# Kernel tuning notes

Hardware: AMD Instinct MI355X
Metric: run time of the kernel (lower is better)

The kernel has to match this reference:

```python
import jax, jax.numpy as jnp
import numpy as np

B, S, H = 32768, 16, 16  # batch, seq_len, G_hiddensize (code requires H == S and H == latent_dim == 16)
LATENT = 16
DISC_DIMS = [(1, 32), (32, 16), (16, 8), (8, 16), (16, 32)]


def setup_inputs() -> dict:
    key = jax.random.key(0)
    ks = iter(jax.random.split(key, 64))
    def p(shape, scale=0.1):
        return (jax.random.normal(next(ks), shape, dtype=jnp.float32) * scale)
    inp = dict(
        values=jax.random.normal(next(ks), (B, S), dtype=jnp.float32),
        masks=jax.random.randint(next(ks), (B, S), 0, 2).astype(jnp.int32),
        g_fwd_Wih=p((4 * H, 1)), g_fwd_Whh=p((4 * H, H)), g_fwd_b=p((4 * H,)),
        g_bwd_Wih=p((4 * H, 1)), g_bwd_Whh=p((4 * H, H)), g_bwd_b=p((4 * H,)),
        imp_W=p((1, H)), imp_b=p((1,)),
        fc_W=p((LATENT, H)), fc_b=p((LATENT,)),
        dec_Wih=p((4 * H, LATENT)), dec_Whh=p((4 * H, H)), dec_b=p((4 * H,)),
        dec_out_W=p((1, H)), dec_out_b=p((1,)),
        disc_out_W=p((1, 32)), disc_out_b=p((1,)),
    )
    for k, (i, h) in enumerate(DISC_DIMS):
        inp[f"d_W_{k}"] = p((4 * h, i))
        inp[f"d_b_{k}"] = p((4 * h,))
    return inp


def lstm_cell(x, h, c, Wih, Whh, b):
    gates = x @ Wih.T + h @ Whh.T + b
    i, f, g, o = jnp.split(gates, 4, axis=-1)
    c = jax.nn.sigmoid(f) * c + jax.nn.sigmoid(i) * jnp.tanh(g)
    h = jax.nn.sigmoid(o) * jnp.tanh(c)
    return h, c


def _forward(values, masks, g_fwd_Wih, g_fwd_Whh, g_fwd_b, g_bwd_Wih, g_bwd_Whh, g_bwd_b,
             imp_W, imp_b, fc_W, fc_b, dec_Wih, dec_Whh, dec_b, dec_out_W, dec_out_b,
             disc_out_W, disc_out_b,
             d_W_0, d_b_0, d_W_1, d_b_1, d_W_2, d_b_2, d_W_3, d_b_3, d_W_4, d_b_4):
    dt = values.dtype
    Bsz = values.shape[0]
    x = values[:, :, None]                     # (B, S, 1)
    m = masks.astype(dt)[:, :, None]           # (B, S, 1)
    # NOTE: torch.flip along axis 2 (size 1) is a no-op, so the bwd cell sees the
    # same (un-reversed) sequence as the fwd cell -- faithfully reproduced here.
    zH = jnp.zeros((Bsz, H), dt)
    h_f, c_f = lstm_cell(jnp.full((Bsz, 1), 128.0, dt), zH, zH, g_fwd_Wih, g_fwd_Whh, g_fwd_b)
    h_b, c_b = lstm_cell(jnp.full((Bsz, 1), -128.0, dt), zH, zH, g_bwd_Wih, g_bwd_Whh, g_bwd_b)

    def gen_step(carry, xm):
        h_f, c_f, h_b, c_b = carry
        x_t, m_t = xm                          # (B,1) each
        cc_f = (1 - m_t) * x_t + m_t * (h_f @ imp_W.T + imp_b)
        cc_b = (1 - m_t) * x_t + m_t * (h_b @ imp_W.T + imp_b)
        h_f, c_f = lstm_cell(cc_f, h_f, c_f, g_fwd_Wih, g_fwd_Whh, g_fwd_b)
        h_b, c_b = lstm_cell(cc_b, h_b, c_b, g_bwd_Wih, g_bwd_Whh, g_bwd_b)
        return (h_f, c_f, h_b, c_b), None

    (h_f, c_f, h_b, c_b), _ = jax.lax.scan(
        gen_step, (h_f, c_f, h_b, c_b),
        (jnp.transpose(x, (1, 0, 2)), jnp.transpose(m, (1, 0, 2))))
    h = h_f + h_b                               # (B, H), H == S
    imputations = h.reshape(Bsz, S, 1)
    imputed = imputations * (1 - m) + x * m      # (B, S, 1)

    # Discriminator: torch calls each LSTMCell WITHOUT state every timestep, so
    # hidden/cell start at zero each call -> purely feedforward per (batch, t).
    # W_hh @ 0 == 0, so only W_ih and the combined bias matter. Vectorize over B*S.
    inp = imputed.reshape(Bsz * S, 1)
    for W, b in ((d_W_0, d_b_0), (d_W_1, d_b_1), (d_W_2, d_b_2), (d_W_3, d_b_3), (d_W_4, d_b_4)):
        gates = inp @ W.T + b
        i, f, g, o = jnp.split(gates, 4, axis=-1)
        cc = jax.nn.sigmoid(i) * jnp.tanh(g)
        inp = jax.nn.sigmoid(o) * jnp.tanh(cc)
    disc_output = (inp @ disc_out_W.T + disc_out_b).reshape(Bsz, S, 1)

    latent = h @ fc_W.T + fc_b                  # (B, 16)

    # Decoder: ignores latent values (only uses batch size); start token = 128s.
    hd = cd = jnp.zeros((Bsz, H), dt)
    hd, cd = lstm_cell(jnp.full((Bsz, LATENT), 128.0, dt), hd, cd, dec_Wih, dec_Whh, dec_b)

    def dec_step(carry, _):
        hd, cd = carry
        hd, cd = lstm_cell(cd, hd, cd, dec_Wih, dec_Whh, dec_b)
        return (hd, cd), hd @ dec_out_W.T + dec_out_b

    _, outs = jax.lax.scan(dec_step, (hd, cd), None, length=S)  # (S, B, 1)
    reconstructed = jnp.transpose(outs, (1, 0, 2))
    return imputed, disc_output, latent, reconstructed


def reference(values, masks, g_fwd_Wih, g_fwd_Whh, g_fwd_b, g_bwd_Wih, g_bwd_Whh, g_bwd_b,
              imp_W, imp_b, fc_W, fc_b, dec_Wih, dec_Whh, dec_b, dec_out_W, dec_out_b,
              disc_out_W, disc_out_b,
              d_W_0, d_b_0, d_W_1, d_b_1, d_W_2, d_b_2, d_W_3, d_b_3, d_W_4, d_b_4):
    return _forward(values, masks, g_fwd_Wih, g_fwd_Whh, g_fwd_b, g_bwd_Wih, g_bwd_Whh, g_bwd_b,
                    imp_W, imp_b, fc_W, fc_b, dec_Wih, dec_Whh, dec_b, dec_out_W, dec_out_b,
                    disc_out_W, disc_out_b,
                    d_W_0, d_b_0, d_W_1, d_b_1, d_W_2, d_b_2, d_W_3, d_b_3, d_W_4, d_b_4)
```

## Files before the change

### kernel.cpp

```cpp
#include <hip/hip_runtime.h>

#define BB 32768
#define BS (BB*16)

typedef __attribute__((ext_vector_type(8))) short bf8v;
typedef __attribute__((ext_vector_type(4))) float f4v;

#define RECO 64
#define TAB  128
#define NTAB 2049
#define HFO  8448
#define HBO  (HFO+BS)

#define PW0 0
#define PB0 96
#define PW1 192
#define PB1 1920
#define PW2 1968
#define PB2 2448
#define PW3 2472
#define PB3 3048
#define PW4 3096
#define PB4 5016
#define POW 5112
#define POB 5144
#define PNU 5148

#define SMF 2580

#define NSCAN 256
#define NTABB 129

__device__ __forceinline__ float sigm(float x){
    return __builtin_amdgcn_rcpf(1.f + __expf(-x));
}
__device__ __forceinline__ float tanh_f(float x){
    return 1.f - 2.f * __builtin_amdgcn_rcpf(1.f + __expf(2.f * x));
}
__device__ __forceinline__ float dunit(float gi, float gg, float go){
    return sigm(go) * tanh_f(sigm(gi) * tanh_f(gg));
}
__device__ __forceinline__ unsigned short f2bf(float f){
    union { float f; unsigned int i; } v; v.f = f;
    unsigned int x = v.i;
    unsigned int r = x + 0x7fffu + ((x >> 16) & 1u);
    return (unsigned short)(r >> 16);
}
__device__ __forceinline__ float bfu(unsigned short s){
    union { unsigned u; float f; } v; v.u = ((unsigned)s) << 16; return v.f;
}
__device__ __forceinline__ float bflo(unsigned p){
    union { unsigned u; float f; } v; v.u = p << 16; return v.f;
}
__device__ __forceinline__ float bfhi(unsigned p){
    union { unsigned u; float f; } v; v.u = p & 0xffff0000u; return v.f;
}

struct P29 { const float* p[29]; };

__device__ __forceinline__ bf8v makeB(const float* Whh, const float* Wih,
                                      int row, int quad)
{
    bf8v B = {0,0,0,0,0,0,0,0};
    if (quad < 2) {
        const float4* p = (const float4*)(Whh + row*16 + quad*8);
        float4 a0 = p[0], a1 = p[1];
        B[0]=(short)f2bf(a0.x); B[1]=(short)f2bf(a0.y);
        B[2]=(short)f2bf(a0.z); B[3]=(short)f2bf(a0.w);
        B[4]=(short)f2bf(a1.x); B[5]=(short)f2bf(a1.y);
        B[6]=(short)f2bf(a1.z); B[7]=(short)f2bf(a1.w);
    } else if (quad == 2) {
        B[0] = (short)f2bf(Wih[row]);
    }
    return B;
}

__global__ __launch_bounds__(256, 1)
void k_main(P29 a, const int* __restrict__ masks, float* __restrict__ ws)
{
    __shared__ __align__(16) float smem[SMF];
    int tid = threadIdx.x;

    if (blockIdx.x < NSCAN) {
        int lane = tid & 63;
        int wv   = tid >> 6;
        int m    = lane & 15;
        int quad = lane >> 4;
        int dir  = (int)(blockIdx.x >= 128);
        int b0   = (blockIdx.x & 127) * 256 + wv * 64;

        const float* __restrict__ Wih = a.p[2 + 3*dir];
        const float* __restrict__ Whh = a.p[3 + 3*dir];
        const float* __restrict__ bia = a.p[4 + 3*dir];

        bf8v Ai = makeB(Whh, Wih, m,      quad);
        bf8v Af = makeB(Whh, Wih, 16+m,   quad);
        bf8v Ag = makeB(Whh, Wih, 32+m,   quad);
        bf8v Ao = makeB(Whh, Wih, 48+m,   quad);
        bf8v Ap = {0,0,0,0,0,0,0,0};
        if (quad < 2) {
            const float4* p = (const float4*)(a.p[8] + quad*8);
            float4 a0 = p[0], a1 = p[1];
            Ap[0]=(short)f2bf(a0.x); Ap[1]=(short)f2bf(a0.y);
            Ap[2]=(short)f2bf(a0.z); Ap[3]=(short)f2bf(a0.w);
            Ap[4]=(short)f2bf(a1.x); Ap[5]=(short)f2bf(a1.y);
            Ap[6]=(short)f2bf(a1.z); Ap[7]=(short)f2bf(a1.w);
        }
        float impb = a.p[9][0];
        const f4v cz = {0.f, 0.f, 0.f, 0.f};

        f4v cbi, cbf, cbg, cbo;
        {
            float4 t;
            t = *(const float4*)(bia +      quad*4); cbi = (f4v){t.x,t.y,t.z,t.w};
            t = *(const float4*)(bia + 16 + quad*4); cbf = (f4v){t.x,t.y,t.z,t.w};
            t = *(const float4*)(bia + 32 + quad*4); cbg = (f4v){t.x,t.y,t.z,t.w};
            t = *(const float4*)(bia + 48 + quad*4); cbo = (f4v){t.x,t.y,t.z,t.w};
        }

        float sgn = dir ? -128.f : 128.f;
        float c[4][4], hl[4][4];
        {
            float4 wI = *(const float4*)(Wih +      quad*4);
            float4 wG = *(const float4*)(Wih + 32 + quad*4);
            float4 wO = *(const float4*)(Wih + 48 + quad*4);
            float wIv[4] = {wI.x, wI.y, wI.z, wI.w};
            float wGv[4] = {wG.x, wG.y, wG.z, wG.w};
            float wOv[4] = {wO.x, wO.y, wO.z, wO.w};
            #pragma unroll
            for (int r = 0; r < 4; r++) {
                float gi0 = sgn*wIv[r] + cbi[r];
                float gg0 = sgn*wGv[r] + cbg[r];
                float go0 = sgn*wOv[r] + cbo[r];
                float c0 = sigm(gi0) * tanh_f(gg0);
                float h0 = sigm(go0) * tanh_f(c0);
                #pragma unroll
                for (int s = 0; s < 4; s++) { c[s][r] = c0; hl[s][r] = h0; }
            }
        }
        unsigned u01[4], u23[4];
        #pragma unroll
        for (int s = 0; s < 4; s++) {
            asm("v_cvt_pk_bf16_f32 %0, %1, %2" : "=v"(u01[s]) : "v"(hl[s][0]), "v"(hl[s][1]));
            asm("v_cvt_pk_bf16_f32 %0, %1, %2" : "=v"(u23[s]) : "v"(hl[s][2]), "v"(hl[s][3]));
        }

        int pa0 = ((m + quad*32)      & 63) << 2;
        int pa1 = ((m + quad*32 + 16) & 63) << 2;

        const float* xr[4];
        const int*   mr[4];
        #pragma unroll
        for (int s = 0; s < 4; s++) {
            xr[s] = a.p[0] + (size_t)(b0 + 16*s + m) * 16;
            mr[s] = masks  + (size_t)(b0 + 16*s + m) * 16;
        }

        #pragma unroll 1
        for (int t4 = 0; t4 < 4; t4++) {
            float xa[4][4];
            int   ma[4][4];
            #pragma unroll
            for (int s = 0; s < 4; s++) {
                float4 xv = *(const float4*)(xr[s] + t4*4);
                int4   mv = *(const int4*)(mr[s] + t4*4);
                xa[s][0]=xv.x; xa[s][1]=xv.y; xa[s][2]=xv.z; xa[s][3]=xv.w;
                ma[s][0]=mv.x; ma[s][1]=mv.y; ma[s][2]=mv.z; ma[s][3]=mv.w;
            }
            #pragma unroll
            for (int j = 0; j < 4; j++) {
                union U4 { int i[4]; bf8v v; } B[4];
                #pragma unroll
                for (int s = 0; s < 4; s++) {
                    int w0 = __builtin_amdgcn_ds_bpermute(pa0, (int)u01[s]);
                    int w1 = __builtin_amdgcn_ds_bpermute(pa0, (int)u23[s]);
                    int w2 = __builtin_amdgcn_ds_bpermute(pa1, (int)u01[s]);
                    int w3 = __builtin_amdgcn_ds_bpermute(pa1, (int)u23[s]);
                    bool hi2 = quad >= 2;
                    B[s].i[0] = hi2 ? 0 : w0;
                    B[s].i[1] = hi2 ? 0 : w1;
                    B[s].i[2] = hi2 ? 0 : w2;
                    B[s].i[3] = hi2 ? 0 : w3;
                }
                #pragma unroll
                for (int s = 0; s < 4; s++) {
                    f4v dimp = __builtin_amdgcn_mfma_f32_16x16x32_bf16(Ap, B[s].v, cz, 0, 0, 0);
                    float cc = ma[s][j] ? (dimp[0] + impb) : xa[s][j];
                    unsigned ccw;
                    asm("v_cvt_pk_bf16_f32 %0, %1, %2" : "=v"(ccw) : "v"(cc), "v"(0.f));
                    if (quad == 2) B[s].i[0] = (int)ccw;
                    f4v di  = __builtin_amdgcn_mfma_f32_16x16x32_bf16(Ai, B[s].v, cbi, 0, 0, 0);
                    f4v df_ = __builtin_amdgcn_mfma_f32_16x16x32_bf16(Af, B[s].v, cbf, 0, 0, 0);
                    f4v dg  = __builtin_amdgcn_mfma_f32_16x16x32_bf16(Ag, B[s].v, cbg, 0, 0, 0);
                    f4v dO  = __builtin_amdgcn_mfma_f32_16x16x32_bf16(Ao, B[s].v, cbo, 0, 0, 0);
                    #pragma unroll
                    for (int r = 0; r < 4; r++) {
                        float cn = sigm(df_[r])*c[s][r] + sigm(di[r])*tanh_f(dg[r]);
                        c[s][r] = cn;
                        hl[s][r] = sigm(dO[r])*tanh_f(cn);
                    }
                    asm("v_cvt_pk_bf16_f32 %0, %1, %2" : "=v"(u01[s]) : "v"(hl[s][0]), "v"(hl[s][1]));
                    asm("v_cvt_pk_bf16_f32 %0, %1, %2" : "=v"(u23[s]) : "v"(hl[s][2]), "v"(hl[s][3]));
                }
            }
        }
        float* outp = ws + HFO + (size_t)dir*BS + (size_t)b0*16;
        #pragma unroll
        for (int s = 0; s < 4; s++)
            #pragma unroll
            for (int r = 0; r < 4; r++)
                outp[(16*s + m)*16 + quad*4 + r] = hl[s][r];
        return;
    }

    if (blockIdx.x < NSCAN + NTABB) {
        unsigned short* wl = (unsigned short*)smem;
#define STAGE(WS, BSi, h, K, padK, wdst, bdst) \
    { const float* Wp = a.p[WS]; const float* Bp2 = a.p[BSi]; \
      for (int i = tid; i < 3*(h)*(K); i += 256){ \
        int r = i/(K), k = i - r*(K); int g = r/(h), u0 = r - g*(h); \
        int sr = (g==0? u0 : (g==1? 2*(h)+u0 : 3*(h)+u0)); \
        wl[(wdst) + r*(padK) + k] = f2bf(Wp[sr*(K) + k]); } \
      for (int i = tid; i < 3*(h); i += 256){ \
        int g = i/(h), u0 = i - g*(h); \
        int sr = (g==0? u0 : (g==1? 2*(h)+u0 : 3*(h)+u0)); \
        wl[(bdst) + i] = f2bf(Bp2[sr]); } }
        STAGE(19, 20, 32,  1,  1, PW0, PB0)
        STAGE(21, 22, 16, 32, 36, PW1, PB1)
        STAGE(23, 24,  8, 16, 20, PW2, PB2)
        STAGE(25, 26, 16,  8, 12, PW3, PB3)
        STAGE(27, 28, 32, 16, 20, PW4, PB4)
#undef STAGE
        { const float* s = a.p[17]; for (int i = tid; i < 32; i += 256) wl[POW+i] = f2bf(s[i]); }
        if (tid == 0) wl[POB] = f2bf(a.p[18][0]);
        __syncthreads();
        int u = tid & 15;
        int gbase = (tid & 63) & 48;
        int gid = (blockIdx.x - NSCAN) * 16 + (tid >> 4);
        const uint2* w2 = (const uint2*)wl;
        float xin = -8.f + (float)gid * (1.f/128.f);
        float lo = dunit(xin*bfu(wl[PW0+u])    + bfu(wl[PB0+u]),
                         xin*bfu(wl[PW0+32+u]) + bfu(wl[PB0+32+u]),
                         xin*bfu(wl[PW0+64+u]) + bfu(wl[PB0+64+u]));
        float hi = dunit(xin*bfu(wl[PW0+16+u]) + bfu(wl[PB0+16+u]),
                         xin*bfu(wl[PW0+48+u]) + bfu(wl[PB0+48+u]),
                         xin*bfu(wl[PW0+80+u]) + bfu(wl[PB0+80+u]));
        float A0[32];
        #pragma unroll
        for (int k = 0; k < 16; k++) { A0[k] = __shfl(lo, gbase+k); A0[16+k] = __shfl(hi, gbase+k); }
        float gi = bfu(wl[PB1+u]), gg = bfu(wl[PB1+16+u]), go = bfu(wl[PB1+32+u]);
        int bi_ = (PW1 + u*36)>>2, bg_ = (PW1 + (16+u)*36)>>2, bo_ = (PW1 + (32+u)*36)>>2;
        #pragma unroll
        for (int q = 0; q < 8; q++) {
            uint2 wi = w2[bi_+q], wg = w2[bg_+q], wo = w2[bo_+q];
            float b0=A0[4*q], b1=A0[4*q+1], b2=A0[4*q+2], b3=A0[4*q+3];
            gi += b0*bflo(wi.x) + b1*bfhi(wi.x) + b2*bflo(wi.y) + b3*bfhi(wi.y);
            gg += b0*bflo(wg.x) + b1*bfhi(wg.x) + b2*bflo(wg.y) + b3*bfhi(wg.y);
            go += b0*bflo(wo.x) + b1*bfhi(wo.x) + b2*bflo(wo.y) + b3*bfhi(wo.y);
        }
        float a1 = dunit(gi, gg, go);
        float A1[16];
        #pragma unroll
        for (int k = 0; k < 16; k++) A1[k] = __shfl(a1, gbase+k);
        int v = u & 7;
        gi = bfu(wl[PB2+v]); gg = bfu(wl[PB2+8+v]); go = bfu(wl[PB2+16+v]);
        bi_ = (PW2 + v*20)>>2; bg_ = (PW2 + (8+v)*20)>>2; bo_ = (PW2 + (16+v)*20)>>2;
        #pragma unroll
        for (int q = 0; q < 4; q++) {
            uint2 wi = w2[bi_+q], wg = w2[bg_+q], wo = w2[bo_+q];
            float b0=A1[4*q], b1=A1[4*q+1], b2=A1[4*q+2], b3=A1[4*q+3];
            gi += b0*bflo(wi.x) + b1*bfhi(wi.x) + b2*bflo(wi.y) + b3*bfhi(wi.y);
            gg += b0*bflo(wg.x) + b1*bfhi(wg.x) + b2*bflo(wg.y) + b3*bfhi(wg.y);
            go += b0*bflo(wo.x) + b1*bfhi(wo.x) + b2*bflo(wo.y) + b3*bfhi(wo.y);
        }
        float a2 = dunit(gi, gg, go);
        float A2[8];
        #pragma unroll
        for (int k = 0; k < 8; k++) A2[k] = __shfl(a2, gbase+k);
        gi = bfu(wl[PB3+u]); gg = bfu(wl[PB3+16+u]); go = bfu(wl[PB3+32+u]);
        bi_ = (PW3 + u*12)>>2; bg_ = (PW3 + (16+u)*12)>>2; bo_ = (PW3 + (32+u)*12)>>2;
        #pragma unroll
        for (int q = 0; q < 2; q++) {
            uint2 wi = w2[bi_+q], wg = w2[bg_+q], wo = w2[bo_+q];
            float b0=A2[4*q], b1=A2[4*q+1], b2=A2[4*q+2], b3=A2[4*q+3];
            gi += b0*bflo(wi.x) + b1*bfhi(wi.x) + b2*bflo(wi.y) + b3*bfhi(wi.y);
            gg += b0*bflo(wg.x) + b1*bfhi(wg.x) + b2*bflo(wg.y) + b3*bfhi(wg.y);
            go += b0*bflo(wo.x) + b1*bfhi(wo.x) + b2*bflo(wo.y) + b3*bfhi(wo.y);
        }
        float a3 = dunit(gi, gg, go);
        float A3[16];
        #pragma unroll
        for (int k = 0; k < 16; k++) A3[k] = __shfl(a3, gbase+k);
        float part;
        {
            float g0i = bfu(wl[PB4+u]),    g0g = bfu(wl[PB4+32+u]), g0o = bfu(wl[PB4+64+u]);
            float g1i = bfu(wl[PB4+16+u]), g1g = bfu(wl[PB4+48+u]), g1o = bfu(wl[PB4+80+u]);
            int c0i = (PW4 + u*20)>>2,      c0g = (PW4 + (32+u)*20)>>2, c0o = (PW4 + (64+u)*20)>>2;
            int c1i = (PW4 + (16+u)*20)>>2, c1g = (PW4 + (48+u)*20)>>2, c1o = (PW4 + (80+u)*20)>>2;
            #pragma unroll
            for (int q = 0; q < 4; q++) {
                float b0=A3[4*q], b1=A3[4*q+1], b2=A3[4*q+2], b3=A3[4*q+3];
                uint2 wi = w2[c0i+q], wg = w2[c0g+q], wo = w2[c0o+q];
                g0i += b0*bflo(wi.x) + b1*bfhi(wi.x) + b2*bflo(wi.y) + b3*bfhi(wi.y);
                g0g += b0*bflo(wg.x) + b1*bfhi(wg.x) + b2*bflo(wg.y) + b3*bfhi(wg.y);
                g0o += b0*bflo(wo.x) + b1*bfhi(wo.x) + b2*bflo(wo.y) + b3*bfhi(wo.y);
                wi = w2[c1i+q]; wg = w2[c1g+q]; wo = w2[c1o+q];
                g1i += b0*bflo(wi.x) + b1*bfhi(wi.x) + b2*bflo(wi.y) + b3*bfhi(wi.y);
                g1g += b0*bflo(wg.x) + b1*bfhi(wg.x) + b2*bflo(wg.y) + b3*bfhi(wg.y);
                g1o += b0*bflo(wo.x) + b1*bfhi(wo.x) + b2*bflo(wo.y) + b3*bfhi(wo.y);
            }
            part = dunit(g0i, g0g, g0o)*bfu(wl[POW+u]) + dunit(g1i, g1g, g1o)*bfu(wl[POW+16+u]);
        }
        part += __shfl_xor(part, 1);
        part += __shfl_xor(part, 2);
        part += __shfl_xor(part, 4);
        part += __shfl_xor(part, 8);
        if (u == 0 && gid < NTAB) ws[TAB + gid] = part + bfu(wl[POB]);
        return;
    }

    {
        float* dh = smem;
        float* dc = smem + 16;
        const float* Wih = a.p[12];
        const float* Whh = a.p[13];
        const float* bb  = a.p[14];
        const float* oW  = a.p[15];
        const float* ob  = a.p[16];
        float wii[16], wff[16], wgg[16], woo[16];
        float vii[16], vff[16], vgg[16], voo[16];
        float bi_r=0, bf_r=0, bg_r=0, bo_r=0;
        if (tid < 16) {
            int uu = tid;
            #pragma unroll
            for (int k = 0; k < 16; k++) {
                wii[k]=Wih[uu*16+k];      vii[k]=Whh[uu*16+k];
                wff[k]=Wih[(16+uu)*16+k]; vff[k]=Whh[(16+uu)*16+k];
                wgg[k]=Wih[(32+uu)*16+k]; vgg[k]=Whh[(32+uu)*16+k];
                woo[k]=Wih[(48+uu)*16+k]; voo[k]=Whh[(48+uu)*16+k];
            }
            bi_r=bb[uu]; bf_r=bb[16+uu]; bg_r=bb[32+uu]; bo_r=bb[48+uu];
            float gi = bi_r, gg = bg_r, go = bo_r;
            #pragma unroll
            for (int k = 0; k < 16; k++) {
                gi += 128.f * wii[k];
                gg += 128.f * wgg[k];
                go += 128.f * woo[k];
            }
            float cd0 = sigm(gi) * tanh_f(gg);
            dc[tid] = cd0; dh[tid] = sigm(go) * tanh_f(cd0);
        }
        __syncthreads();
        for (int t = 0; t < 16; t++) {
            float rx[16], rh[16], cold = 0.f;
            if (tid < 16) {
                #pragma unroll
                for (int k = 0; k < 16; k++) { rx[k] = dc[k]; rh[k] = dh[k]; }
                cold = dc[tid];
            }
            __syncthreads();
            if (tid < 16) {
                float gi = bi_r, gf = bf_r, gg = bg_r, go = bo_r;
                #pragma unroll
                for (int k = 0; k < 16; k++) {
                    gi += rx[k]*wii[k] + rh[k]*vii[k];
                    gf += rx[k]*wff[k] + rh[k]*vff[k];
                    gg += rx[k]*wgg[k] + rh[k]*vgg[k];
                    go += rx[k]*woo[k] + rh[k]*voo[k];
                }
                float cn = sigm(gf)*cold + sigm(gi)*tanh_f(gg);
                dc[tid] = cn; dh[tid] = sigm(go)*tanh_f(cn);
            }
            __syncthreads();
            if (tid == 0) {
                float o = ob[0];
                #pragma unroll
                for (int k = 0; k < 16; k++) o += dh[k] * oW[k];
                ws[RECO + t] = o;
            }
            __syncthreads();
        }
    }
}

__global__ __launch_bounds__(256) void k_post(P29 a, const int* __restrict__ masks,
                                              const float* __restrict__ ws,
                                              float* __restrict__ out)
{
    __shared__ float tab[NTAB];
    __shared__ __align__(16) float fw[256];
    __shared__ __align__(16) float rec[16];
    __shared__ float fb[16];
    int tid = threadIdx.x;
    for (int i = tid; i < NTAB; i += 256) tab[i] = ws[TAB + i];
    fw[tid] = a.p[10][tid];
    if (tid < 16) { fb[tid] = a.p[11][tid]; rec[tid] = ws[RECO + tid]; }
    __syncthreads();
    int T = blockIdx.x * 256 + tid;
    int b = T >> 2;
    int q = T & 3;
    int tq = q * 4;
    const float4* hf4 = (const float4*)(ws + HFO + (size_t)b*16);
    const float4* hb4 = (const float4*)(ws + HBO + (size_t)b*16);
    float4 s0, s1, s2, s3;
    {
        float4 f0=hf4[0], f1=hf4[1], f2=hf4[2], f3=hf4[3];
        float4 g0=hb4[0], g1=hb4[1], g2=hb4[2], g3=hb4[3];
        s0 = make_float4(f0.x+g0.x, f0.y+g0.y, f0.z+g0.z, f0.w+g0.w);
        s1 = make_float4(f1.x+g1.x, f1.y+g1.y, f1.z+g1.z, f1.w+g1.w);
        s2 = make_float4(f2.x+g2.x, f2.y+g2.y, f2.z+g2.z, f2.w+g2.w);
        s3 = make_float4(f3.x+g3.x, f3.y+g3.y, f3.z+g3.z, f3.w+g3.w);
    }
    float4 hq = (q==0) ? s0 : (q==1) ? s1 : (q==2) ? s2 : s3;
    float4 xv = *(const float4*)(a.p[0] + (size_t)b*16 + tq);
    int4   mv = *(const int4*)(masks + (size_t)b*16 + tq);
    float impv[4];
    impv[0] = mv.x ? xv.x : hq.x;
    impv[1] = mv.y ? xv.y : hq.y;
    impv[2] = mv.z ? xv.z : hq.z;
    impv[3] = mv.w ? xv.w : hq.w;
    float latv[4];
    #pragma unroll
    for (int j = 0; j < 4; j++) {
        int t = tq + j;
        const float4* wr = (const float4*)(fw + t*16);
        float4 w0=wr[0], w1=wr[1], w2=wr[2], w3=wr[3];
        float l = fb[t];
        l += s0.x*w0.x + s0.y*w0.y + s0.z*w0.z + s0.w*w0.w;
        l += s1.x*w1.x + s1.y*w1.y + s1.z*w1.z + s1.w*w1.w;
        l += s2.x*w2.x + s2.y*w2.y + s2.z*w2.z + s2.w*w2.w;
        l += s3.x*w3.x + s3.y*w3.y + s3.z*w3.z + s3.w*w3.w;
        latv[j] = l;
    }
    float dv[4];
    #pragma unroll
    for (int j = 0; j < 4; j++) {
        float xx = fminf(fmaxf(impv[j], -8.f), 8.f);
        float f = (xx + 8.f) * 128.f;
        float fi = floorf(f);
        int i = (int)fi; i = i > NTAB-2 ? NTAB-2 : i;
        float w = f - fi;
        dv[j] = fmaf(w, tab[i+1] - tab[i], tab[i]);
    }
    float4 rv = ((const float4*)rec)[q];
    size_t eo = (size_t)b*16 + tq;
    *(float4*)(out + eo)        = make_float4(impv[0], impv[1], impv[2], impv[3]);
    *(float4*)(out + BS + eo)   = make_float4(dv[0], dv[1], dv[2], dv[3]);
    *(float4*)(out + 2*BS + eo) = make_float4(latv[0], latv[1], latv[2], latv[3]);
    *(float4*)(out + 3*BS + eo) = rv;
}

extern "C" void kernel_launch(void* const* d_in, const int* in_sizes, int n_in,
                              void* d_out, int out_size, void* d_ws, size_t ws_size,
                              hipStream_t stream)
{
    float* ws = (float*)d_ws;
    P29 a;
    for (int i = 0; i < 29; i++) a.p[i] = (const float*)d_in[i];
    const int* masks = (const int*)d_in[1];
    k_main<<<NSCAN + NTABB + 1, 256, 0, stream>>>(a, masks, ws);
    k_post<<<(BB*4)/256, 256, 0, stream>>>(a, masks, ws, (float*)d_out);
}
```

Before: 151.2 us.

## Reorder MFMA K-dimension to feed hidden state directly without bpermute shuffles

Rearranges the K-dimension layout of the LSTM weight fragments so each lane's own packed hidden values (quad*4..quad*4+3) line up with the MFMA B-operand. The four ds_bpermute cross-lane shuffles per sequence slice per timestep are removed, and the input/imputed value is placed in slot 4 for quad 0. This shortens the recurrent critical path, at the cost of a sparser K-packing and reliance on the MFMA operand layout being matched exactly.

```diff
diff --git a/kernel.cpp b/kernel.cpp
--- a/kernel.cpp
+++ b/kernel.cpp
@@ -58,21 +58,15 @@
 
 struct P29 { const float* p[29]; };
 
-__device__ __forceinline__ bf8v makeB(const float* Whh, const float* Wih,
+__device__ __forceinline__ bf8v makeA(const float* Whh, const float* Wih,
                                       int row, int quad)
 {
-    bf8v B = {0,0,0,0,0,0,0,0};
-    if (quad < 2) {
-        const float4* p = (const float4*)(Whh + row*16 + quad*8);
-        float4 a0 = p[0], a1 = p[1];
-        B[0]=(short)f2bf(a0.x); B[1]=(short)f2bf(a0.y);
-        B[2]=(short)f2bf(a0.z); B[3]=(short)f2bf(a0.w);
-        B[4]=(short)f2bf(a1.x); B[5]=(short)f2bf(a1.y);
-        B[6]=(short)f2bf(a1.z); B[7]=(short)f2bf(a1.w);
-    } else if (quad == 2) {
-        B[0] = (short)f2bf(Wih[row]);
-    }
-    return B;
+    bf8v A = {0,0,0,0,0,0,0,0};
+    float4 a0 = *(const float4*)(Whh + row*16 + quad*4);
+    A[0]=(short)f2bf(a0.x); A[1]=(short)f2bf(a0.y);
+    A[2]=(short)f2bf(a0.z); A[3]=(short)f2bf(a0.w);
+    if (quad == 0) A[4] = (short)f2bf(Wih[row]);
+    return A;
 }
 
 __global__ __launch_bounds__(256, 1)
@@ -93,18 +87,15 @@
         const float* __restrict__ Whh = a.p[3 + 3*dir];
         const float* __restrict__ bia = a.p[4 + 3*dir];
 
-        bf8v Ai = makeB(Whh, Wih, m,      quad);
-        bf8v Af = makeB(Whh, Wih, 16+m,   quad);
-        bf8v Ag = makeB(Whh, Wih, 32+m,   quad);
-        bf8v Ao = makeB(Whh, Wih, 48+m,   quad);
+        bf8v Ai = makeA(Whh, Wih, m,      quad);
+        bf8v Af = makeA(Whh, Wih, 16+m,   quad);
+        bf8v Ag = makeA(Whh, Wih, 32+m,   quad);
+        bf8v Ao = makeA(Whh, Wih, 48+m,   quad);
         bf8v Ap = {0,0,0,0,0,0,0,0};
-        if (quad < 2) {
-            const float4* p = (const float4*)(a.p[8] + quad*8);
-            float4 a0 = p[0], a1 = p[1];
+        {
+            float4 a0 = *(const float4*)(a.p[8] + quad*4);
             Ap[0]=(short)f2bf(a0.x); Ap[1]=(short)f2bf(a0.y);
             Ap[2]=(short)f2bf(a0.z); Ap[3]=(short)f2bf(a0.w);
-            Ap[4]=(short)f2bf(a1.x); Ap[5]=(short)f2bf(a1.y);
-            Ap[6]=(short)f2bf(a1.z); Ap[7]=(short)f2bf(a1.w);
         }
         float impb = a.p[9][0];
         const f4v cz = {0.f, 0.f, 0.f, 0.f};
@@ -145,9 +136,6 @@
             asm("v_cvt_pk_bf16_f32 %0, %1, %2" : "=v"(u23[s]) : "v"(hl[s][2]), "v"(hl[s][3]));
         }
 
-        int pa0 = ((m + quad*32)      & 63) << 2;
-        int pa1 = ((m + quad*32 + 16) & 63) << 2;
-
         const float* xr[4];
         const int*   mr[4];
         #pragma unroll
@@ -155,6 +143,7 @@
             xr[s] = a.p[0] + (size_t)(b0 + 16*s + m) * 16;
             mr[s] = masks  + (size_t)(b0 + 16*s + m) * 16;
         }
+        bool q0 = (quad == 0);
 
         #pragma unroll 1
         for (int t4 = 0; t4 < 4; t4++) {
@@ -169,30 +158,22 @@
             }
             #pragma unroll
             for (int j = 0; j < 4; j++) {
-                union U4 { int i[4]; bf8v v; } B[4];
                 #pragma unroll
                 for (int s = 0; s < 4; s++) {
-                    int w0 = __builtin_amdgcn_ds_bpermute(pa0, (int)u01[s]);
-                    int w1 = __builtin_amdgcn_ds_bpermute(pa0, (int)u23[s]);
-                    int w2 = __builtin_amdgcn_ds_bpermute(pa1, (int)u01[s]);
-                    int w3 = __builtin_amdgcn_ds_bpermute(pa1, (int)u23[s]);
-                    bool hi2 = quad >= 2;
-                    B[s].i[0] = hi2 ? 0 : w0;
-                    B[s].i[1] = hi2 ? 0 : w1;
-                    B[s].i[2] = hi2 ? 0 : w2;
-                    B[s].i[3] = hi2 ? 0 : w3;
-                }
-                #pragma unroll
-                for (int s = 0; s < 4; s++) {
-                    f4v dimp = __builtin_amdgcn_mfma_f32_16x16x32_bf16(Ap, B[s].v, cz, 0, 0, 0);
+                    union U4 { int i[4]; bf8v v; } B;
+                    B.i[0] = (int)u01[s];
+                    B.i[1] = (int)u23[s];
+                    B.i[2] = 0;
+                    B.i[3] = 0;
+                    f4v dimp = __builtin_amdgcn_mfma_f32_16x16x32_bf16(Ap, B.v, cz, 0, 0, 0);
                     float cc = ma[s][j] ? (dimp[0] + impb) : xa[s][j];
                     unsigned ccw;
                     asm("v_cvt_pk_bf16_f32 %0, %1, %2" : "=v"(ccw) : "v"(cc), "v"(0.f));
-                    if (quad == 2) B[s].i[0] = (int)ccw;
-                    f4v di  = __builtin_amdgcn_mfma_f32_16x16x32_bf16(Ai, B[s].v, cbi, 0, 0, 0);
-                    f4v df_ = __builtin_amdgcn_mfma_f32_16x16x32_bf16(Af, B[s].v, cbf, 0, 0, 0);
-                    f4v dg  = __builtin_amdgcn_mfma_f32_16x16x32_bf16(Ag, B[s].v, cbg, 0, 0, 0);
-                    f4v dO  = __builtin_amdgcn_mfma_f32_16x16x32_bf16(Ao, B[s].v, cbo, 0, 0, 0);
+                    if (q0) B.i[2] = (int)ccw;
+                    f4v di  = __builtin_amdgcn_mfma_f32_16x16x32_bf16(Ai, B.v, cbi, 0, 0, 0);
+                    f4v df_ = __builtin_amdgcn_mfma_f32_16x16x32_bf16(Af, B.v, cbf, 0, 0, 0);
+                    f4v dg  = __builtin_amdgcn_mfma_f32_16x16x32_bf16(Ag, B.v, cbg, 0, 0, 0);
+                    f4v dO  = __builtin_amdgcn_mfma_f32_16x16x32_bf16(Ao, B.v, cbo, 0, 0, 0);
                     #pragma unroll
                     for (int r = 0; r < 4; r++) {
                         float cn = sigm(df_[r])*c[s][r] + sigm(di[r])*tanh_f(dg[r]);
```

Result: no change. 151.8 us (+0.4%).
